# Optimization experiments

Measured on AMD Instinct MI355X. Metric: run time of the kernel, lower is better.

Reference implementation:

```python
import jax, jax.numpy as jnp
import numpy as np

N, C, H, W = 8, 64, 128, 128
K2 = 9  # 3x3 kernel
BN_EPS = 1e-5


def conv3x3(x, w):
    # x: [N,Ci,H,W], w: [Co,Ci,3,3], stride 1, padding 1, dilation 1
    return jax.lax.conv_general_dilated(
        x, w, window_strides=(1, 1), padding=((1, 1), (1, 1)),
        dimension_numbers=('NCHW', 'OIHW', 'NCHW'))


def deform_conv3x3(x, offset, w):
    # torchvision deform_conv2d v1 (no mask), stride 1, pad 1, dil 1, 1 group.
    # offset: [N, 2*K2, H, W] ordered (dy, dx) per kernel tap.
    n, c, h, wd = x.shape
    off = offset.reshape(n, K2, 2, h, wd)
    k = jnp.arange(3) - 1  # kernel tap displacements with pad=1
    ky, kx = jnp.meshgrid(k, k, indexing='ij')
    ky = ky.reshape(K2).astype(x.dtype)
    kx = kx.reshape(K2).astype(x.dtype)
    ys = jnp.arange(h, dtype=x.dtype)
    xs = jnp.arange(wd, dtype=x.dtype)
    # sampling positions: [N, K2, H, W]
    py = ys[None, None, :, None] + ky[None, :, None, None] + off[:, :, 0]
    px = xs[None, None, None, :] + kx[None, :, None, None] + off[:, :, 1]
    y0f = jnp.floor(py)
    x0f = jnp.floor(px)
    wy1 = py - y0f
    wx1 = px - x0f
    y0 = y0f.astype(jnp.int32)
    x0 = x0f.astype(jnp.int32)
    xflat = x.reshape(n, c, h * wd)

    def corner(yc, xc, wgt):
        valid = ((yc >= 0) & (yc < h) & (xc >= 0) & (xc < wd)).astype(x.dtype)
        idx = jnp.clip(yc, 0, h - 1) * wd + jnp.clip(xc, 0, wd - 1)  # [N,K2,H,W]
        gath = jax.vmap(lambda xf, i: jnp.take(xf, i.reshape(-1), axis=1)
                        .reshape(c, K2, h, wd))(xflat, idx)  # [N,C,K2,H,W]
        return gath * (wgt * valid)[:, None]

    samp = (corner(y0, x0, (1 - wy1) * (1 - wx1))
            + corner(y0, x0 + 1, (1 - wy1) * wx1)
            + corner(y0 + 1, x0, wy1 * (1 - wx1))
            + corner(y0 + 1, x0 + 1, wy1 * wx1))  # [N,C,K2,H,W]
    return jnp.einsum('nckhw,ock->nohw', samp, w.reshape(w.shape[0], c, K2))


def setup_inputs() -> dict:
    key = jax.random.key(0)
    ks = jax.random.split(key, 5)
    x = jax.random.normal(ks[0], (N, C, H, W), dtype=jnp.float32)
    # small offset-conv weights so predicted offsets stay within a few pixels
    w_off = jax.random.normal(ks[1], (2 * K2 + 9, C, 3, 3), dtype=jnp.float32) * 0.01
    w_def = jax.random.normal(ks[2], (C, C, 3, 3), dtype=jnp.float32) * (1.0 / np.sqrt(C * 9))
    w1 = jax.random.normal(ks[3], (K2, C, 3, 3), dtype=jnp.float32) * (1.0 / np.sqrt(C * 9))
    gamma = jnp.ones((K2,), jnp.float32)
    beta = jnp.zeros((K2,), jnp.float32)
    mean = jnp.zeros((K2,), jnp.float32)
    var = jnp.ones((K2,), jnp.float32)
    return {"x": x, "w_off": w_off, "w_def": w_def, "w1": w1,
            "gamma": gamma, "beta": beta, "mean": mean, "var": var}


def reference(x, w_off, w_def, w1, gamma, beta, mean, var):
    off_filter = conv3x3(x, w_off)            # [N, 27, H, W]
    offset = off_filter[:, :2 * K2]           # [N, 18, H, W]
    filt = off_filter[:, -K2:]                # [N, 9, H, W]
    out = deform_conv3x3(x, offset, w_def)    # [N, C, H, W]
    xr = x + out
    h = conv3x3(xr, w1)                       # [N, 9, H, W]
    # BatchNorm2d (inference form with running stats)
    h = (h - mean[None, :, None, None]) * jax.lax.rsqrt(var[None, :, None, None] + BN_EPS)
    h = h * gamma[None, :, None, None] + beta[None, :, None, None]
    h = jnp.maximum(h, 0.0)
    return (h, filt)
```

## Files before the change

### kernel.cpp

```cpp
#include <hip/hip_runtime.h>
#include <cmath>

#define H_ 128
#define W_ 128
#define HW_ 16384
#define C_ 64
#define N_ 8
#define BN_EPS 1e-5f

typedef __attribute__((ext_vector_type(8))) short short8;
typedef __attribute__((ext_vector_type(4))) float float4_;

__device__ inline short f2bf(float f) {
    unsigned u = __builtin_bit_cast(unsigned, f);
    u += 0x7fffu + ((u >> 16) & 1u);
    return (short)(u >> 16);
}
__device__ inline float bf2f(short s) {
    unsigned u = ((unsigned)(unsigned short)s) << 16;
    return __builtin_bit_cast(float, u);
}

#define XR8_OFS    0
#define WDEFB_OFS  16777216
#define BT27_OFS   16850944
#define BT9_OFS    16888320

#define PS_ 402
#define OS_ 260

__global__ __launch_bounds__(256) void prep_w(
    const float* __restrict__ w_off, const float* __restrict__ w_def,
    const float* __restrict__ w1, short* __restrict__ wdefB,
    short* __restrict__ bt27, short* __restrict__ bt9)
{
    int i = blockIdx.x * 256 + threadIdx.x;
    if (i < 36864) {
        int o = i / 576, r = i - o*576, t = r >> 6, c = r & 63;
        wdefB[i] = f2bf(w_def[o*576 + c*9 + t]);
    } else if (i < 36864 + 18688) {
        int j = i - 36864;
        int oc = j / 584, K = j - oc*584;
        float v = 0.f;
        if (oc < 27 && K < 576) { int t = K >> 6, c = K & 63; v = w_off[oc*576 + c*9 + t]; }
        bt27[j] = f2bf(v);
    } else if (i < 36864 + 18688 + 9344) {
        int j = i - 36864 - 18688;
        int oc = j / 584, K = j - oc*584;
        float v = 0.f;
        if (oc < 9 && K < 576) { int t = K >> 6, c = K & 63; v = w1[oc*576 + c*9 + t]; }
        bt9[j] = f2bf(v);
    }
}

__global__ __launch_bounds__(256, 2) void fused_off_deform(
    const float* __restrict__ x, const short8* __restrict__ btg27,
    const short8* __restrict__ wdefB, float* __restrict__ filt_out,
    short* __restrict__ xr8s)
{
    __shared__ short8 patch[8*PS_];
    __shared__ float  offs[18*OS_];
    const int tid = threadIdx.x;
    const int bx = blockIdx.x, by = blockIdx.y, n = blockIdx.z;
    const int lane = tid & 63, wid = tid >> 6;
    const int q = lane >> 4, col = lane & 15;
    const int r0 = by*16 - 2, c0 = bx*16 - 2;
    const float* xb = x + (size_t)n * C_ * HW_;

    for (int i = tid; i < 3200; i += 256) {
        int c8 = i / 400, r = i - c8*400;
        int py = r / 20, px = r - py*20;
        int gy = r0 + py, gx = c0 + px;
        short8 v = {0,0,0,0,0,0,0,0};
        if ((unsigned)gy < 128u && (unsigned)gx < 128u) {
            const float* xp = xb + (size_t)(c8*8)*HW_ + gy*W_ + gx;
            #pragma unroll
            for (int j = 0; j < 8; j++) v[j] = f2bf(xp[j*HW_]);
        }
        patch[c8*PS_ + py*20 + px] = v;
    }
    __syncthreads();

    {
        float4_ a27[4][2];
        #pragma unroll
        for (int i = 0; i < 4; i++) {
            a27[i][0] = (float4_){0.f,0.f,0.f,0.f};
            a27[i][1] = (float4_){0.f,0.f,0.f,0.f};
        }
        #pragma unroll 2
        for (int k0 = 0; k0 < 18; k0++) {
            int t = k0 >> 1;
            int dy = t/3, dx = t - dy*3;
            int c8 = (k0 & 1)*4 + q;
            short8 b0 = btg27[col*73 + k0*4 + q];
            short8 b1 = btg27[(16 + col)*73 + k0*4 + q];
            #pragma unroll
            for (int i = 0; i < 4; i++) {
                int mt = wid*4 + i;
                short8 a = patch[c8*PS_ + (mt + dy + 1)*20 + (col + dx + 1)];
                a27[i][0] = __builtin_amdgcn_mfma_f32_16x16x32_bf16(a, b0, a27[i][0], 0,0,0);
                a27[i][1] = __builtin_amdgcn_mfma_f32_16x16x32_bf16(a, b1, a27[i][1], 0,0,0);
            }
        }
        #pragma unroll
        for (int i = 0; i < 4; i++) {
            int mt = wid*4 + i;
            #pragma unroll
            for (int nt = 0; nt < 2; nt++) {
                int oc = nt*16 + col;
                if (oc < 18) {
                    *(float4_*)&offs[oc*OS_ + mt*16 + q*4] = a27[i][nt];
                } else if (oc < 27) {
                    int pix0 = (by*16 + mt)*W_ + bx*16 + q*4;
                    *(float4_*)&filt_out[((size_t)n*9 + (oc-18))*HW_ + pix0] = a27[i][nt];
                }
            }
        }
    }
    __syncthreads();

    float4_ acc[4][4];
    #pragma unroll
    for (int i = 0; i < 4; i++)
        #pragma unroll
        for (int nt = 0; nt < 4; nt++) acc[i][nt] = (float4_){0.f,0.f,0.f,0.f};

    #pragma unroll 1
    for (int t = 0; t < 9; t++) {
        const int dy = t/3 - 1, dx = (t - (t/3)*3) - 1;
        short8 afrag[4][2];
        #pragma unroll
        for (int i = 0; i < 4; i++) {
            const int row = wid*4 + i;
            const int gy = by*16 + row, gxc = bx*16 + col;
            float oy = offs[(2*t)*OS_ + row*16 + col];
            float ox = offs[(2*t+1)*OS_ + row*16 + col];
            float py = (float)(gy + dy) + oy;
            float px = (float)(gxc + dx) + ox;
            float y0f = floorf(py), x0f = floorf(px);
            float wy1 = py - y0f, wx1 = px - x0f;
            float wy0 = 1.f - wy1, wx0 = 1.f - wx1;
            int y0 = (int)y0f, x0 = (int)x0f;
            int y1 = y0 + 1,   x1 = x0 + 1;
            float vy0 = ((unsigned)y0 < (unsigned)H_) ? 1.f : 0.f;
            float vy1 = ((unsigned)y1 < (unsigned)H_) ? 1.f : 0.f;
            float vx0 = ((unsigned)x0 < (unsigned)W_) ? 1.f : 0.f;
            float vx1 = ((unsigned)x1 < (unsigned)W_) ? 1.f : 0.f;
            float w00 = wy0*wx0*vy0*vx0, w01 = wy0*wx1*vy0*vx1;
            float w10 = wy1*wx0*vy1*vx0, w11 = wy1*wx1*vy1*vx1;
            int cy0 = min(max(y0, 0), H_-1), cy1 = min(max(y1, 0), H_-1);
            int cx0 = min(max(x0, 0), W_-1), cx1 = min(max(x1, 0), W_-1);
            int ly0 = cy0 - r0, ly1 = cy1 - r0;
            int lx0 = cx0 - c0, lx1 = cx1 - c0;
            bool inp = ((unsigned)ly0 < 20u) & ((unsigned)ly1 < 20u)
                     & ((unsigned)lx0 < 20u) & ((unsigned)lx1 < 20u);
            #pragma unroll
            for (int ks = 0; ks < 2; ks++) {
                const int c8 = ks*4 + q;
                short8 a;
                if (inp) {
                    const short8* pl = &patch[c8*PS_];
                    short8 p00 = pl[ly0*20 + lx0], p01 = pl[ly0*20 + lx1];
                    short8 p10 = pl[ly1*20 + lx0], p11 = pl[ly1*20 + lx1];
                    #pragma unroll
                    for (int j = 0; j < 8; j++) {
                        float s = bf2f(p00[j])*w00 + bf2f(p01[j])*w01
                                + bf2f(p10[j])*w10 + bf2f(p11[j])*w11;
                        a[j] = f2bf(s);
                    }
                } else {
                    const float* xg = xb + (size_t)(c8*8)*HW_;
                    #pragma unroll
                    for (int j = 0; j < 8; j++) {
                        const float* xj = xg + (size_t)j*HW_;
                        float s = xj[cy0*W_+cx0]*w00 + xj[cy0*W_+cx1]*w01
                                + xj[cy1*W_+cx0]*w10 + xj[cy1*W_+cx1]*w11;
                        a[j] = f2bf(s);
                    }
                }
                afrag[i][ks] = a;
            }
        }
        #pragma unroll
        for (int ks = 0; ks < 2; ks++) {
            #pragma unroll
            for (int nt = 0; nt < 4; nt++) {
                short8 b = wdefB[(size_t)(nt*16 + col)*72 + t*8 + ks*4 + q];
                #pragma unroll
                for (int i = 0; i < 4; i++)
                    acc[i][nt] = __builtin_amdgcn_mfma_f32_16x16x32_bf16(
                        afrag[i][ks], b, acc[i][nt], 0,0,0);
            }
        }
    }

    const short* ps = (const short*)patch;
    short* xout = xr8s + (size_t)n*8*HW_*8;
    #pragma unroll
    for (int i = 0; i < 4; i++) {
        const int row = wid*4 + i;
        const int gy = by*16 + row;
        #pragma unroll
        for (int nt = 0; nt < 4; nt++) {
            const int o = nt*16 + col;
            #pragma unroll
            for (int reg = 0; reg < 4; reg++) {
                const int m = q*4 + reg;
                const int pix = gy*W_ + bx*16 + m;
                float r = bf2f(ps[(((o>>3)*PS_ + (row+2)*20 + (m+2)) << 3) + (o & 7)]);
                xout[((size_t)(o>>3)*HW_ + pix)*8 + (o & 7)] = f2bf(acc[i][nt][reg] + r);
            }
        }
    }
}

__global__ __launch_bounds__(256) void conv9_mfma(
    const short8* __restrict__ xr8, const short* __restrict__ bt_g,
    const float* __restrict__ gamma, const float* __restrict__ beta,
    const float* __restrict__ mean, const float* __restrict__ var,
    float* __restrict__ out)
{
    __shared__ short8 patch[8*325];
    __shared__ short8 btl[16*73];
    const int tid = threadIdx.x;
    const int bx = blockIdx.x, by = blockIdx.y, n = blockIdx.z;

    for (int i = tid; i < 1168; i += 256) btl[i] = ((const short8*)bt_g)[i];
    for (int i = tid; i < 2592; i += 256) {
        int c8 = i / 324, r = i - c8*324;
        int py = r / 18, px = r - py*18;
        int gy = by*16 - 1 + py, gx = bx*16 - 1 + px;
        short8 v = {0,0,0,0,0,0,0,0};
        if ((unsigned)gy < 128u && (unsigned)gx < 128u)
            v = xr8[(size_t)(n*8 + c8)*HW_ + gy*W_ + gx];
        patch[c8*325 + py*18 + px] = v;
    }
    __syncthreads();

    const int lane = tid & 63, wid = tid >> 6;
    const int q = lane >> 4, col = lane & 15;
    float4_ acc[4];
    #pragma unroll
    for (int i = 0; i < 4; i++) acc[i] = (float4_){0.f,0.f,0.f,0.f};

    #pragma unroll 2
    for (int k0 = 0; k0 < 18; k0++) {
        int t = k0 >> 1;
        int dy = t/3, dx = t - dy*3;
        int c8 = (k0 & 1)*4 + q;
        short8 b0 = btl[col*73 + k0*4 + q];
        #pragma unroll
        for (int i = 0; i < 4; i++) {
            int mt = wid*4 + i;
            short8 a = patch[c8*325 + (mt + dy)*18 + (col + dx)];
            acc[i] = __builtin_amdgcn_mfma_f32_16x16x32_bf16(a, b0, acc[i], 0,0,0);
        }
    }

    float sc = 0.f, sh = 0.f;
    if (col < 9) {
        sc = gamma[col] * rsqrtf(var[col] + BN_EPS);
        sh = beta[col] - mean[col] * sc;
    }
    #pragma unroll
    for (int i = 0; i < 4; i++) {
        int mt = wid*4 + i;
        if (col < 9) {
            int pix0 = (by*16 + mt)*W_ + bx*16 + q*4;
            float4_ v;
            #pragma unroll
            for (int reg = 0; reg < 4; reg++)
                v[reg] = fmaxf(fmaf(acc[i][reg], sc, sh), 0.f);
            *(float4_*)&out[((size_t)n*9 + col)*HW_ + pix0] = v;
        }
    }
}

extern "C" void kernel_launch(void* const* d_in, const int* in_sizes, int n_in,
                              void* d_out, int out_size, void* d_ws, size_t ws_size,
                              hipStream_t stream)
{
    const float* x     = (const float*)d_in[0];
    const float* w_off = (const float*)d_in[1];
    const float* w_def = (const float*)d_in[2];
    const float* w1    = (const float*)d_in[3];
    const float* gamma = (const float*)d_in[4];
    const float* beta  = (const float*)d_in[5];
    const float* mean  = (const float*)d_in[6];
    const float* var   = (const float*)d_in[7];
    float* out = (float*)d_out;

    char* ws = (char*)d_ws;
    short8* xr8     = (short8*)(ws + XR8_OFS);
    short*  wdefB   = (short*)(ws + WDEFB_OFS);
    short*  bt27    = (short*)(ws + BT27_OFS);
    short*  bt9     = (short*)(ws + BT9_OFS);

    float* h_out    = out;
    float* filt_out = out + (size_t)N_ * 9 * HW_;

    prep_w<<<dim3(254), dim3(256), 0, stream>>>(w_off, w_def, w1, wdefB, bt27, bt9);

    dim3 cgrid(8, 8, 8);
    fused_off_deform<<<cgrid, dim3(256), 0, stream>>>(
        x, (const short8*)bt27, (const short8*)wdefB, filt_out, (short*)xr8);
    conv9_mfma<<<cgrid, dim3(256), 0, stream>>>(xr8, bt9, gamma, beta, mean, var, h_out);
}
```

Baseline: 163.0 us.

## Keep offset-conv results in registers and redistribute via ds_bpermute instead of LDS

The offset conv MFMA now swaps its operands so each lane holds per-pixel results for output channels, and offsets are shuffled across lanes with ds_bpermute instead of being staged through a shared-memory offsets array. This removes the offs LDS buffer and a block barrier, which lowers LDS use and may allow higher occupancy. Tap 8 is handled separately because its offsets sit in the second accumulator. Other changes: bf16 packing uses the paired conversion intrinsic, validity masks fold directly into the bilinear weights, and conv9 reads weights from global memory instead of staging them in LDS. The risks are extra cross-lane permutes in the tap loop and uncached-LDS weight loads in conv9.

```diff
diff --git a/kernel.cpp b/kernel.cpp
--- a/kernel.cpp
+++ b/kernel.cpp
@@ -1,4 +1,5 @@
 #include <hip/hip_runtime.h>
+#include <hip/hip_bf16.h>
 #include <cmath>
 
 #define H_ 128
@@ -10,6 +11,7 @@
 
 typedef __attribute__((ext_vector_type(8))) short short8;
 typedef __attribute__((ext_vector_type(4))) float float4_;
+typedef __attribute__((ext_vector_type(4))) unsigned uint4_;
 
 __device__ inline short f2bf(float f) {
     unsigned u = __builtin_bit_cast(unsigned, f);
@@ -20,6 +22,16 @@
     unsigned u = ((unsigned)(unsigned short)s) << 16;
     return __builtin_bit_cast(float, u);
 }
+__device__ inline unsigned pkbf2(float a, float b) {
+    __hip_bfloat162 h = __float22bfloat162_rn(make_float2(a, b));
+    unsigned u;
+    __builtin_memcpy(&u, &h, 4);
+    return u;
+}
+__device__ inline float bperm_f(int addr, float v) {
+    return __builtin_bit_cast(float,
+        __builtin_amdgcn_ds_bpermute(addr, __builtin_bit_cast(int, v)));
+}
 
 #define XR8_OFS    0
 #define WDEFB_OFS  16777216
@@ -27,7 +39,6 @@
 #define BT9_OFS    16888320
 
 #define PS_ 402
-#define OS_ 260
 
 __global__ __launch_bounds__(256) void prep_w(
     const float* __restrict__ w_off, const float* __restrict__ w_def,
@@ -59,7 +70,6 @@
     short* __restrict__ xr8s)
 {
     __shared__ short8 patch[8*PS_];
-    __shared__ float  offs[18*OS_];
     const int tid = threadIdx.x;
     const int bx = blockIdx.x, by = blockIdx.y, n = blockIdx.z;
     const int lane = tid & 63, wid = tid >> 6;
@@ -71,54 +81,50 @@
         int c8 = i / 400, r = i - c8*400;
         int py = r / 20, px = r - py*20;
         int gy = r0 + py, gx = c0 + px;
-        short8 v = {0,0,0,0,0,0,0,0};
+        uint4_ u = (uint4_){0u,0u,0u,0u};
         if ((unsigned)gy < 128u && (unsigned)gx < 128u) {
             const float* xp = xb + (size_t)(c8*8)*HW_ + gy*W_ + gx;
-            #pragma unroll
-            for (int j = 0; j < 8; j++) v[j] = f2bf(xp[j*HW_]);
-        }
-        patch[c8*PS_ + py*20 + px] = v;
+            u[0] = pkbf2(xp[0],      xp[HW_]);
+            u[1] = pkbf2(xp[2*HW_],  xp[3*HW_]);
+            u[2] = pkbf2(xp[4*HW_],  xp[5*HW_]);
+            u[3] = pkbf2(xp[6*HW_],  xp[7*HW_]);
+        }
+        patch[c8*PS_ + py*20 + px] = __builtin_bit_cast(short8, u);
     }
     __syncthreads();
 
-    {
-        float4_ a27[4][2];
-        #pragma unroll
-        for (int i = 0; i < 4; i++) {
-            a27[i][0] = (float4_){0.f,0.f,0.f,0.f};
-            a27[i][1] = (float4_){0.f,0.f,0.f,0.f};
-        }
-        #pragma unroll 2
-        for (int k0 = 0; k0 < 18; k0++) {
-            int t = k0 >> 1;
-            int dy = t/3, dx = t - dy*3;
-            int c8 = (k0 & 1)*4 + q;
-            short8 b0 = btg27[col*73 + k0*4 + q];
-            short8 b1 = btg27[(16 + col)*73 + k0*4 + q];
-            #pragma unroll
-            for (int i = 0; i < 4; i++) {
-                int mt = wid*4 + i;
-                short8 a = patch[c8*PS_ + (mt + dy + 1)*20 + (col + dx + 1)];
-                a27[i][0] = __builtin_amdgcn_mfma_f32_16x16x32_bf16(a, b0, a27[i][0], 0,0,0);
-                a27[i][1] = __builtin_amdgcn_mfma_f32_16x16x32_bf16(a, b1, a27[i][1], 0,0,0);
-            }
-        }
+    float4_ a27[2][4];
+    #pragma unroll
+    for (int m = 0; m < 2; m++)
+        #pragma unroll
+        for (int i = 0; i < 4; i++) a27[m][i] = (float4_){0.f,0.f,0.f,0.f};
+
+    #pragma unroll 2
+    for (int k0 = 0; k0 < 18; k0++) {
+        int t = k0 >> 1;
+        int dy = t/3, dx = t - dy*3;
+        int c8 = (k0 & 1)*4 + q;
+        short8 w0 = btg27[col*73 + k0*4 + q];
+        short8 w1 = btg27[(16 + col)*73 + k0*4 + q];
         #pragma unroll
         for (int i = 0; i < 4; i++) {
             int mt = wid*4 + i;
-            #pragma unroll
-            for (int nt = 0; nt < 2; nt++) {
-                int oc = nt*16 + col;
-                if (oc < 18) {
-                    *(float4_*)&offs[oc*OS_ + mt*16 + q*4] = a27[i][nt];
-                } else if (oc < 27) {
-                    int pix0 = (by*16 + mt)*W_ + bx*16 + q*4;
-                    *(float4_*)&filt_out[((size_t)n*9 + (oc-18))*HW_ + pix0] = a27[i][nt];
-                }
-            }
-        }
-    }
-    __syncthreads();
+            short8 p = patch[c8*PS_ + (mt + dy + 1)*20 + (col + dx + 1)];
+            a27[0][i] = __builtin_amdgcn_mfma_f32_16x16x32_bf16(w0, p, a27[0][i], 0,0,0);
+            a27[1][i] = __builtin_amdgcn_mfma_f32_16x16x32_bf16(w1, p, a27[1][i], 0,0,0);
+        }
+    }
+
+    #pragma unroll
+    for (int i = 0; i < 4; i++) {
+        int prow = by*16 + wid*4 + i;
+        #pragma unroll
+        for (int reg = 0; reg < 4; reg++) {
+            int oc = 16 + q*4 + reg;
+            if (oc >= 18 && oc < 27)
+                filt_out[((size_t)n*9 + (oc-18))*HW_ + prow*W_ + bx*16 + col] = a27[1][i][reg];
+        }
+    }
 
     float4_ acc[4][4];
     #pragma unroll
@@ -126,29 +132,27 @@
         #pragma unroll
         for (int nt = 0; nt < 4; nt++) acc[i][nt] = (float4_){0.f,0.f,0.f,0.f};
 
-    #pragma unroll 1
-    for (int t = 0; t < 9; t++) {
-        const int dy = t/3 - 1, dx = (t - (t/3)*3) - 1;
+    const int col4 = col*4;
+    const int gxc = bx*16 + col;
+
+    auto tap = [&](int t, int dy, int dx, const float* oy, const float* ox) {
         short8 afrag[4][2];
         #pragma unroll
         for (int i = 0; i < 4; i++) {
-            const int row = wid*4 + i;
-            const int gy = by*16 + row, gxc = bx*16 + col;
-            float oy = offs[(2*t)*OS_ + row*16 + col];
-            float ox = offs[(2*t+1)*OS_ + row*16 + col];
-            float py = (float)(gy + dy) + oy;
-            float px = (float)(gxc + dx) + ox;
+            const int gy = by*16 + wid*4 + i;
+            float py = (float)(gy + dy) + oy[i];
+            float px = (float)(gxc + dx) + ox[i];
             float y0f = floorf(py), x0f = floorf(px);
             float wy1 = py - y0f, wx1 = px - x0f;
             float wy0 = 1.f - wy1, wx0 = 1.f - wx1;
             int y0 = (int)y0f, x0 = (int)x0f;
             int y1 = y0 + 1,   x1 = x0 + 1;
-            float vy0 = ((unsigned)y0 < (unsigned)H_) ? 1.f : 0.f;
-            float vy1 = ((unsigned)y1 < (unsigned)H_) ? 1.f : 0.f;
-            float vx0 = ((unsigned)x0 < (unsigned)W_) ? 1.f : 0.f;
-            float vx1 = ((unsigned)x1 < (unsigned)W_) ? 1.f : 0.f;
-            float w00 = wy0*wx0*vy0*vx0, w01 = wy0*wx1*vy0*vx1;
-            float w10 = wy1*wx0*vy1*vx0, w11 = wy1*wx1*vy1*vx1;
+            float wy0v = ((unsigned)y0 < (unsigned)H_) ? wy0 : 0.f;
+            float wy1v = ((unsigned)y1 < (unsigned)H_) ? wy1 : 0.f;
+            float wx0v = ((unsigned)x0 < (unsigned)W_) ? wx0 : 0.f;
+            float wx1v = ((unsigned)x1 < (unsigned)W_) ? wx1 : 0.f;
+            float w00 = wy0v*wx0v, w01 = wy0v*wx1v;
+            float w10 = wy1v*wx0v, w11 = wy1v*wx1v;
             int cy0 = min(max(y0, 0), H_-1), cy1 = min(max(y1, 0), H_-1);
             int cx0 = min(max(x0, 0), W_-1), cx1 = min(max(x1, 0), W_-1);
             int ly0 = cy0 - r0, ly1 = cy1 - r0;
@@ -158,28 +162,31 @@
             #pragma unroll
             for (int ks = 0; ks < 2; ks++) {
                 const int c8 = ks*4 + q;
-                short8 a;
+                uint4_ u;
                 if (inp) {
                     const short8* pl = &patch[c8*PS_];
                     short8 p00 = pl[ly0*20 + lx0], p01 = pl[ly0*20 + lx1];
                     short8 p10 = pl[ly1*20 + lx0], p11 = pl[ly1*20 + lx1];
+                    float s[8];
                     #pragma unroll
-                    for (int j = 0; j < 8; j++) {
-                        float s = bf2f(p00[j])*w00 + bf2f(p01[j])*w01
-                                + bf2f(p10[j])*w10 + bf2f(p11[j])*w11;
-                        a[j] = f2bf(s);
-                    }
+                    for (int j = 0; j < 8; j++)
+                        s[j] = bf2f(p00[j])*w00 + bf2f(p01[j])*w01
+                             + bf2f(p10[j])*w10 + bf2f(p11[j])*w11;
+                    u[0] = pkbf2(s[0],s[1]); u[1] = pkbf2(s[2],s[3]);
+                    u[2] = pkbf2(s[4],s[5]); u[3] = pkbf2(s[6],s[7]);
                 } else {
                     const float* xg = xb + (size_t)(c8*8)*HW_;
+                    float s[8];
                     #pragma unroll
                     for (int j = 0; j < 8; j++) {
                         const float* xj = xg + (size_t)j*HW_;
-                        float s = xj[cy0*W_+cx0]*w00 + xj[cy0*W_+cx1]*w01
-                                + xj[cy1*W_+cx0]*w10 + xj[cy1*W_+cx1]*w11;
-                        a[j] = f2bf(s);
+                        s[j] = xj[cy0*W_+cx0]*w00 + xj[cy0*W_+cx1]*w01
+                             + xj[cy1*W_+cx0]*w10 + xj[cy1*W_+cx1]*w11;
                     }
+                    u[0] = pkbf2(s[0],s[1]); u[1] = pkbf2(s[2],s[3]);
+                    u[2] = pkbf2(s[4],s[5]); u[3] = pkbf2(s[6],s[7]);
                 }
-                afrag[i][ks] = a;
+                afrag[i][ks] = __builtin_bit_cast(short8, u);
             }
         }
         #pragma unroll
@@ -193,6 +200,32 @@
                         afrag[i][ks], b, acc[i][nt], 0,0,0);
             }
         }
+    };
+
+    {
+        float oy[4], ox[4];
+        #pragma unroll
+        for (int i = 0; i < 4; i++) {
+            oy[i] = bperm_f(col4, a27[1][i][0]);
+            ox[i] = bperm_f(col4, a27[1][i][1]);
+        }
+        tap(8, 1, 1, oy, ox);
+    }
+    #pragma unroll 1
+    for (int t = 0; t < 8; t++) {
+        const int addr = ((t >> 1) << 6) + col4;
+        float oy[4], ox[4];
+        #pragma unroll
+        for (int i = 0; i < 4; i++) {
+            float oyA = bperm_f(addr, a27[0][i][0]);
+            float oyB = bperm_f(addr, a27[0][i][2]);
+            float oxA = bperm_f(addr, a27[0][i][1]);
+            float oxB = bperm_f(addr, a27[0][i][3]);
+            oy[i] = (t & 1) ? oyB : oyA;
+            ox[i] = (t & 1) ? oxB : oxA;
+        }
+        int dy = t/3 - 1, dx = (t - (t/3)*3) - 1;
+        tap(t, dy, dx, oy, ox);
     }
 
     const short* ps = (const short*)patch;
@@ -216,17 +249,15 @@
 }
 
 __global__ __launch_bounds__(256) void conv9_mfma(
-    const short8* __restrict__ xr8, const short* __restrict__ bt_g,
+    const short8* __restrict__ xr8, const short8* __restrict__ btg,
     const float* __restrict__ gamma, const float* __restrict__ beta,
     const float* __restrict__ mean, const float* __restrict__ var,
     float* __restrict__ out)
 {
     __shared__ short8 patch[8*325];
-    __shared__ short8 btl[16*73];
     const int tid = threadIdx.x;
     const int bx = blockIdx.x, by = blockIdx.y, n = blockIdx.z;
 
-    for (int i = tid; i < 1168; i += 256) btl[i] = ((const short8*)bt_g)[i];
     for (int i = tid; i < 2592; i += 256) {
         int c8 = i / 324, r = i - c8*324;
         int py = r / 18, px = r - py*18;
@@ -249,7 +280,7 @@
         int t = k0 >> 1;
         int dy = t/3, dx = t - dy*3;
         int c8 = (k0 & 1)*4 + q;
-        short8 b0 = btl[col*73 + k0*4 + q];
+        short8 b0 = btg[col*73 + k0*4 + q];
         #pragma unroll
         for (int i = 0; i < 4; i++) {
             int mt = wid*4 + i;
@@ -305,5 +336,6 @@
     dim3 cgrid(8, 8, 8);
     fused_off_deform<<<cgrid, dim3(256), 0, stream>>>(
         x, (const short8*)bt27, (const short8*)wdefB, filt_out, (short*)xr8);
-    conv9_mfma<<<cgrid, dim3(256), 0, stream>>>(xr8, bt9, gamma, beta, mean, var, h_out);
-}
+    conv9_mfma<<<cgrid, dim3(256), 0, stream>>>(
+        xr8, (const short8*)bt9, gamma, beta, mean, var, h_out);
+}
```

Result: faster. 157.2 us (-3.6%).
